# Kernel optimization log

Measured on AMD Instinct MI355X. Metric: run time of the kernel, lower is better.

Reference implementation:

```python
import jax, jax.numpy as jnp
import numpy as np

EMBED_SIZE = 512
SCALE = EMBED_SIZE ** 0.5  # note: sqrt(embed_size), not sqrt(head_dim), per source


def setup_inputs() -> dict:
    key = jax.random.key(0)
    kq, kk, kv = jax.random.split(key, 3)
    B, H, S, D = 4, 8, 2048, 64
    query = jax.random.normal(kq, (B, H, S, D), dtype=jnp.float32)
    key_t = jax.random.normal(kk, (B, H, S, D), dtype=jnp.float32)
    value = jax.random.normal(kv, (B, S, H, D), dtype=jnp.float32)  # [b, kv_len, h, d]
    return {"query": query, "key": key_t, "value": value}


def reference(query, key, value):
    # scores: [b, h, q, k]
    scores = jnp.einsum('bhqf,bhkf->bhqk', query, key)
    weight = jax.nn.softmax(scores / SCALE, axis=3)
    # value is [b, l, h, d]; output [b, q, h, d]
    out = jnp.einsum('bhql,blhd->bqhd', weight, value)
    return out
```

## Files before the change

### kernel.cpp

```cpp
#include <hip/hip_runtime.h>
#include <stdint.h>

#define NB 4
#define NH 8
#define NS 2048
#define ND 64
#define BQ 128
#define TK 64
#define KP 72
#define NG 2
#define NITG (NS/(TK*NG))
#define SLOT (TK*KP + ND*KP)

typedef __bf16  bf16x8 __attribute__((ext_vector_type(8)));
typedef float   f32x16 __attribute__((ext_vector_type(16)));

__device__ __forceinline__ uint32_t pkbf(float x, float y) {
  uint32_t ax = __builtin_bit_cast(uint32_t, x) + 0x8000u;
  uint32_t ay = __builtin_bit_cast(uint32_t, y) + 0x8000u;
  return __builtin_amdgcn_perm(ay, ax, 0x07060302u);
}
__device__ __forceinline__ unsigned short bfu(float x) {
  return (unsigned short)((__builtin_bit_cast(uint32_t, x) + 0x8000u) >> 16);
}

__global__ __launch_bounds__(512, 4) void fa_fwd(
    const float* __restrict__ Q, const float* __restrict__ K,
    const float* __restrict__ V, float* __restrict__ O)
{
  __shared__ __attribute__((aligned(16))) unsigned short SMEM[NG*2*SLOT];

  const int tid = threadIdx.x, wid = tid>>6, lane = tid&63;
  const int l31 = lane&31, h = lane>>5;
  const int g = wid>>2, qs = wid&3;
  const int tid4 = tid & 255;

  const int bid = blockIdx.x;
  const int logical = (bid & 7)*64 + (bid >> 3);
  const int bh = logical >> 4;
  const int q0 = (logical & 15) * BQ;
  const int b = bh>>3, hh = bh&7;

  const float* Qb = Q + ((size_t)bh*NS + q0)*ND;
  const float* Kb = K + (size_t)bh*NS*ND;
  const float* Vb = V + ((size_t)b*NS*NH + hh)*ND;
  float*       Ob = O + ((size_t)b*NS*NH + hh)*ND;

  const float kSc = 1.44269504088896340736f / 22.6274169979695207808f;

  bf16x8 qf[4];
  {
    const float* qp = Qb + (size_t)(qs*32 + l31)*ND + 8*h;
#pragma unroll
    for (int k=0;k<4;++k){
      float4 a = *(const float4*)(qp + 16*k);
      float4 c = *(const float4*)(qp + 16*k + 4);
      uint4 u = make_uint4(pkbf(a.x*kSc,a.y*kSc), pkbf(a.z*kSc,a.w*kSc),
                           pkbf(c.x*kSc,c.y*kSc), pkbf(c.z*kSc,c.w*kSc));
      qf[k] = __builtin_bit_cast(bf16x8, u);
    }
  }

  const int krow0 = tid4>>3, koct = tid&7;
  const int vq = lane&3, vrow = 16*qs + (lane>>2);

  float4 kst[2][2], vst[4];
  auto load_tile = [&](int kv0){
#pragma unroll
    for (int i=0;i<2;++i){
      const float* kp = Kb + (size_t)(kv0 + krow0 + 32*i)*ND + koct*8;
      kst[i][0] = *(const float4*)kp;
      kst[i][1] = *(const float4*)(kp+4);
    }
    const float* vp = Vb + (size_t)(kv0 + vrow)*(NH*ND) + 4*vq;
#pragma unroll
    for (int j=0;j<4;++j)
      vst[j] = *(const float4*)(vp + 16*j);
  };
  auto store_tile = [&](int buf){
    unsigned short* Kl = SMEM + (size_t)(g*2+buf)*SLOT;
    unsigned short* Vt = Kl + TK*KP;
#pragma unroll
    for (int i=0;i<2;++i){
      uint4 w = make_uint4(pkbf(kst[i][0].x,kst[i][0].y), pkbf(kst[i][0].z,kst[i][0].w),
                           pkbf(kst[i][1].x,kst[i][1].y), pkbf(kst[i][1].z,kst[i][1].w));
      *(uint4*)&Kl[(size_t)(krow0+32*i)*KP + koct*8] = w;
    }
#pragma unroll
    for (int j=0;j<4;++j){
      int d0 = 16*j + 4*vq;
      Vt[(size_t)(d0+0)*KP + vrow] = bfu(vst[j].x);
      Vt[(size_t)(d0+1)*KP + vrow] = bfu(vst[j].y);
      Vt[(size_t)(d0+2)*KP + vrow] = bfu(vst[j].z);
      Vt[(size_t)(d0+3)*KP + vrow] = bfu(vst[j].w);
    }
  };

  load_tile(g*NITG*TK);
  store_tile(0);
  __syncthreads();

  const f32x16 zero = {0,0,0,0,0,0,0,0,0,0,0,0,0,0,0,0};
  f32x16 acc[2] = {zero, zero};
  float lsum = 0.f;

  for (int t=0; t<NITG; ++t){
    const int cur = t&1;
    if (t+1 < NITG) load_tile((g*NITG + t + 1)*TK);

    const unsigned short* Kl = SMEM + (size_t)(g*2+cur)*SLOT;
    const unsigned short* Vt = Kl + TK*KP;

    f32x16 st[2];
    __builtin_amdgcn_s_setprio(1);
#pragma unroll
    for (int tt=0;tt<2;++tt){
      st[tt] = zero;
#pragma unroll
      for (int k=0;k<4;++k){
        bf16x8 kf = *(const bf16x8*)&Kl[(size_t)(32*tt+l31)*KP + 16*k + 8*h];
        st[tt] = __builtin_amdgcn_mfma_f32_32x32x16_bf16(kf, qf[k], st[tt], 0,0,0);
      }
    }
    __builtin_amdgcn_s_setprio(0);

    uint32_t P0[2][4], P1[2][4];
#pragma unroll
    for (int tt=0;tt<2;++tt)
#pragma unroll
      for (int u=0;u<4;++u){
        float p0 = __builtin_amdgcn_exp2f(st[tt][4*u+0]);
        float p1 = __builtin_amdgcn_exp2f(st[tt][4*u+1]);
        float p2 = __builtin_amdgcn_exp2f(st[tt][4*u+2]);
        float p3 = __builtin_amdgcn_exp2f(st[tt][4*u+3]);
        lsum += (p0+p1)+(p2+p3);
        P0[tt][u] = pkbf(p0,p1);
        P1[tt][u] = pkbf(p2,p3);
      }

    uint32_t X0[2][2], X1[2][2];
#pragma unroll
    for (int tt=0;tt<2;++tt)
#pragma unroll
      for (int m=0;m<2;++m){
        uint32_t y0 = h ? P0[tt][2*m] : P0[tt][2*m+1];
        uint32_t y1 = h ? P1[tt][2*m] : P1[tt][2*m+1];
        X0[tt][m] = (uint32_t)__shfl_xor((int)y0, 32, 64);
        X1[tt][m] = (uint32_t)__shfl_xor((int)y1, 32, 64);
      }
    bf16x8 pf[4];
#pragma unroll
    for (int k=0;k<4;++k){
      int tt = k>>1, m = k&1;
      uint32_t lo0 = h ? X0[tt][m]     : P0[tt][2*m];
      uint32_t lo1 = h ? X1[tt][m]     : P1[tt][2*m];
      uint32_t hi0 = h ? P0[tt][2*m+1] : X0[tt][m];
      uint32_t hi1 = h ? P1[tt][2*m+1] : X1[tt][m];
      uint4 u = make_uint4(lo0, lo1, hi0, hi1);
      pf[k] = __builtin_bit_cast(bf16x8, u);
    }

    __builtin_amdgcn_s_setprio(1);
#pragma unroll
    for (int gg=0;gg<2;++gg)
#pragma unroll
      for (int k=0;k<4;++k){
        bf16x8 vf = *(const bf16x8*)&Vt[(size_t)(32*gg+l31)*KP + 16*k + 8*h];
        acc[gg] = __builtin_amdgcn_mfma_f32_32x32x16_bf16(vf, pf[k], acc[gg], 0,0,0);
      }
    __builtin_amdgcn_s_setprio(0);

    if (t+1 < NITG) store_tile(cur^1);
    __syncthreads();
  }

  lsum += __shfl_xor(lsum, 32, 64);
  const int row = qs*32 + l31;
  float* accL = (float*)SMEM;
  float* lsL  = accL + 128*68;

  if (g==1){
#pragma unroll
    for (int gg=0; gg<2; ++gg)
#pragma unroll
      for (int u=0; u<4; ++u){
        float4 o;
        o.x = acc[gg][4*u+0]; o.y = acc[gg][4*u+1];
        o.z = acc[gg][4*u+2]; o.w = acc[gg][4*u+3];
        *(float4*)&accL[(size_t)row*68 + 32*gg + 8*u + 4*h] = o;
      }
    if (h==0) lsL[row] = lsum;
  }
  __syncthreads();
  if (g==0){
    const float inv = 1.0f/(lsum + lsL[row]);
    float* op = Ob + (size_t)(q0 + row)*(NH*ND);
#pragma unroll
    for (int gg=0; gg<2; ++gg)
#pragma unroll
      for (int u=0; u<4; ++u){
        float4 c = *(const float4*)&accL[(size_t)row*68 + 32*gg + 8*u + 4*h];
        float4 o;
        o.x = (acc[gg][4*u+0]+c.x)*inv;
        o.y = (acc[gg][4*u+1]+c.y)*inv;
        o.z = (acc[gg][4*u+2]+c.z)*inv;
        o.w = (acc[gg][4*u+3]+c.w)*inv;
        *(float4*)(op + 32*gg + 8*u + 4*h) = o;
      }
  }
}

extern "C" void kernel_launch(void* const* d_in, const int* in_sizes, int n_in,
                              void* d_out, int out_size, void* d_ws, size_t ws_size,
                              hipStream_t stream) {
  const float* Q = (const float*)d_in[0];
  const float* K = (const float*)d_in[1];
  const float* V = (const float*)d_in[2];
  float* O = (float*)d_out;
  dim3 grid((NS / BQ) * NB * NH);
  hipLaunchKernelGGL(fa_fwd, grid, dim3(512), 0, stream, Q, K, V, O);
}
```

Measured before the change: 149.6 us.

## Double query tile to 256 rows and split K/V staging across thread halves

Raises the query block to 256 rows with 1024-thread blocks, so each shared K/V tile in LDS is reused by 8 query strips per group instead of 4. This halves the global K/V reads and bf16 conversion work per query row. Tile loading is also rebalanced: within each group, one half of the threads stages K and the other half stages transposed V, instead of every thread doing both. The cost is half as many blocks (256), which may hurt load balance or latency hiding, plus larger blocks and a bigger epilogue reduction buffer in LDS.

```diff
diff --git a/kernel.cpp b/kernel.cpp
--- a/kernel.cpp
+++ b/kernel.cpp
@@ -5,7 +5,7 @@
 #define NH 8
 #define NS 2048
 #define ND 64
-#define BQ 128
+#define BQ 256
 #define TK 64
 #define KP 72
 #define NG 2
@@ -24,7 +24,7 @@
   return (unsigned short)((__builtin_bit_cast(uint32_t, x) + 0x8000u) >> 16);
 }
 
-__global__ __launch_bounds__(512, 4) void fa_fwd(
+__global__ __launch_bounds__(1024, 4) void fa_fwd(
     const float* __restrict__ Q, const float* __restrict__ K,
     const float* __restrict__ V, float* __restrict__ O)
 {
@@ -32,13 +32,15 @@
 
   const int tid = threadIdx.x, wid = tid>>6, lane = tid&63;
   const int l31 = lane&31, h = lane>>5;
-  const int g = wid>>2, qs = wid&3;
-  const int tid4 = tid & 255;
+  const int g = wid>>3, qs = wid&7;
+  const int tid9 = tid & 511;
+  const int sub = tid9 >> 8;
+  const int t4 = tid9 & 255;
 
   const int bid = blockIdx.x;
-  const int logical = (bid & 7)*64 + (bid >> 3);
-  const int bh = logical >> 4;
-  const int q0 = (logical & 15) * BQ;
+  const int logical = (bid & 7)*32 + (bid >> 3);
+  const int bh = logical >> 3;
+  const int q0 = (logical & 7) * BQ;
   const int b = bh>>3, hh = bh&7;
 
   const float* Qb = Q + ((size_t)bh*NS + q0)*ND;
@@ -61,38 +63,44 @@
     }
   }
 
-  const int krow0 = tid4>>3, koct = tid&7;
-  const int vq = lane&3, vrow = 16*qs + (lane>>2);
-
-  float4 kst[2][2], vst[4];
+  const int krow0 = t4>>3, koct = t4&7;
+  const int vrow = t4>>2, vq = t4&3;
+
+  float4 stg[4];
   auto load_tile = [&](int kv0){
-#pragma unroll
-    for (int i=0;i<2;++i){
-      const float* kp = Kb + (size_t)(kv0 + krow0 + 32*i)*ND + koct*8;
-      kst[i][0] = *(const float4*)kp;
-      kst[i][1] = *(const float4*)(kp+4);
-    }
-    const float* vp = Vb + (size_t)(kv0 + vrow)*(NH*ND) + 4*vq;
-#pragma unroll
-    for (int j=0;j<4;++j)
-      vst[j] = *(const float4*)(vp + 16*j);
+    if (sub==0){
+      const float* kp = Kb + (size_t)(kv0 + krow0)*ND + koct*8;
+      stg[0] = *(const float4*)kp;
+      stg[1] = *(const float4*)(kp+4);
+      const float* kp2 = kp + 32*ND;
+      stg[2] = *(const float4*)kp2;
+      stg[3] = *(const float4*)(kp2+4);
+    } else {
+      const float* vp = Vb + (size_t)(kv0 + vrow)*(NH*ND) + 4*vq;
+#pragma unroll
+      for (int j=0;j<4;++j)
+        stg[j] = *(const float4*)(vp + 16*j);
+    }
   };
   auto store_tile = [&](int buf){
     unsigned short* Kl = SMEM + (size_t)(g*2+buf)*SLOT;
     unsigned short* Vt = Kl + TK*KP;
-#pragma unroll
-    for (int i=0;i<2;++i){
-      uint4 w = make_uint4(pkbf(kst[i][0].x,kst[i][0].y), pkbf(kst[i][0].z,kst[i][0].w),
-                           pkbf(kst[i][1].x,kst[i][1].y), pkbf(kst[i][1].z,kst[i][1].w));
-      *(uint4*)&Kl[(size_t)(krow0+32*i)*KP + koct*8] = w;
-    }
-#pragma unroll
-    for (int j=0;j<4;++j){
-      int d0 = 16*j + 4*vq;
-      Vt[(size_t)(d0+0)*KP + vrow] = bfu(vst[j].x);
-      Vt[(size_t)(d0+1)*KP + vrow] = bfu(vst[j].y);
-      Vt[(size_t)(d0+2)*KP + vrow] = bfu(vst[j].z);
-      Vt[(size_t)(d0+3)*KP + vrow] = bfu(vst[j].w);
+    if (sub==0){
+      uint4 w0 = make_uint4(pkbf(stg[0].x,stg[0].y), pkbf(stg[0].z,stg[0].w),
+                            pkbf(stg[1].x,stg[1].y), pkbf(stg[1].z,stg[1].w));
+      *(uint4*)&Kl[(size_t)krow0*KP + koct*8] = w0;
+      uint4 w1 = make_uint4(pkbf(stg[2].x,stg[2].y), pkbf(stg[2].z,stg[2].w),
+                            pkbf(stg[3].x,stg[3].y), pkbf(stg[3].z,stg[3].w));
+      *(uint4*)&Kl[(size_t)(krow0+32)*KP + koct*8] = w1;
+    } else {
+#pragma unroll
+      for (int j=0;j<4;++j){
+        int d0 = 16*j + 4*vq;
+        Vt[(size_t)(d0+0)*KP + vrow] = bfu(stg[j].x);
+        Vt[(size_t)(d0+1)*KP + vrow] = bfu(stg[j].y);
+        Vt[(size_t)(d0+2)*KP + vrow] = bfu(stg[j].z);
+        Vt[(size_t)(d0+3)*KP + vrow] = bfu(stg[j].w);
+      }
     }
   };
 
@@ -177,7 +185,7 @@
   lsum += __shfl_xor(lsum, 32, 64);
   const int row = qs*32 + l31;
   float* accL = (float*)SMEM;
-  float* lsL  = accL + 128*68;
+  float* lsL  = accL + 256*68;
 
   if (g==1){
 #pragma unroll
@@ -218,5 +226,5 @@
   const float* V = (const float*)d_in[2];
   float* O = (float*)d_out;
   dim3 grid((NS / BQ) * NB * NH);
-  hipLaunchKernelGGL(fa_fwd, grid, dim3(512), 0, stream, Q, K, V, O);
-}
+  hipLaunchKernelGGL(fa_fwd, grid, dim3(1024), 0, stream, Q, K, V, O);
+}
```

Measured after the change: 170.4 us. +13.9%, slower.

## Precompute bf16 K and transposed bf16 V in a prep kernel

Applied to the files above, without the earlier changes.

Adds a pre-pass kernel that converts K to bf16 and writes V as bf16 transposed into a [b,h,d,s] workspace layout. The attention kernel then loads these half-width tiles with plain 16-byte vector loads and stores them straight to LDS, with no per-tile conversion or scattered transpose stores. This removes repeated fp32 K/V reads and conversion across the 16 query blocks per head. The cost is an extra kernel launch and a full pass over K and V plus workspace writes.

```diff
diff --git a/kernel.cpp b/kernel.cpp
--- a/kernel.cpp
+++ b/kernel.cpp
@@ -24,16 +24,60 @@
   return (unsigned short)((__builtin_bit_cast(uint32_t, x) + 0x8000u) >> 16);
 }
 
+__global__ __launch_bounds__(256) void prep(
+    const float* __restrict__ K, const float* __restrict__ V,
+    unsigned short* __restrict__ Kh, unsigned short* __restrict__ Vth)
+{
+  __shared__ unsigned short T[64*72];
+  const int t = threadIdx.x;
+  const int blk = blockIdx.x;
+  const int bh = blk >> 5, st = blk & 31;
+  const int s0 = st*64;
+  const int b = bh>>3, hh = bh&7;
+
+  {
+    const float* kin = K + ((size_t)bh*NS + s0)*ND + t*16;
+    unsigned short* kout = Kh + ((size_t)bh*NS + s0)*ND + t*16;
+    float4 a0 = ((const float4*)kin)[0], a1 = ((const float4*)kin)[1];
+    float4 a2 = ((const float4*)kin)[2], a3 = ((const float4*)kin)[3];
+    uint4 w0 = make_uint4(pkbf(a0.x,a0.y),pkbf(a0.z,a0.w),pkbf(a1.x,a1.y),pkbf(a1.z,a1.w));
+    uint4 w1 = make_uint4(pkbf(a2.x,a2.y),pkbf(a2.z,a2.w),pkbf(a3.x,a3.y),pkbf(a3.z,a3.w));
+    ((uint4*)kout)[0] = w0; ((uint4*)kout)[1] = w1;
+  }
+
+  {
+    const int vrow = t>>2, vq = t&3;
+    const float* vp = V + (((size_t)b*NS + s0 + vrow)*NH + hh)*ND + 4*vq;
+#pragma unroll
+    for (int j=0;j<4;++j){
+      float4 v = *(const float4*)(vp + 16*j);
+      int d0 = 16*j + 4*vq;
+      T[(size_t)(d0+0)*72 + vrow] = bfu(v.x);
+      T[(size_t)(d0+1)*72 + vrow] = bfu(v.y);
+      T[(size_t)(d0+2)*72 + vrow] = bfu(v.z);
+      T[(size_t)(d0+3)*72 + vrow] = bfu(v.w);
+    }
+  }
+  __syncthreads();
+  {
+    const int dd = t>>2, wq = t&3;
+    unsigned short* vout = Vth + ((size_t)bh*ND + dd)*NS + s0 + 16*wq;
+    uint4 o0 = *(const uint4*)&T[(size_t)dd*72 + 16*wq];
+    uint4 o1 = *(const uint4*)&T[(size_t)dd*72 + 16*wq + 8];
+    ((uint4*)vout)[0] = o0; ((uint4*)vout)[1] = o1;
+  }
+}
+
 __global__ __launch_bounds__(512, 4) void fa_fwd(
-    const float* __restrict__ Q, const float* __restrict__ K,
-    const float* __restrict__ V, float* __restrict__ O)
+    const float* __restrict__ Q, const unsigned short* __restrict__ Kh,
+    const unsigned short* __restrict__ Vth, float* __restrict__ O)
 {
   __shared__ __attribute__((aligned(16))) unsigned short SMEM[NG*2*SLOT];
 
   const int tid = threadIdx.x, wid = tid>>6, lane = tid&63;
   const int l31 = lane&31, h = lane>>5;
   const int g = wid>>2, qs = wid&3;
-  const int tid4 = tid & 255;
+  const int t4 = tid & 255;
 
   const int bid = blockIdx.x;
   const int logical = (bid & 7)*64 + (bid >> 3);
@@ -41,10 +85,10 @@
   const int q0 = (logical & 15) * BQ;
   const int b = bh>>3, hh = bh&7;
 
-  const float* Qb = Q + ((size_t)bh*NS + q0)*ND;
-  const float* Kb = K + (size_t)bh*NS*ND;
-  const float* Vb = V + ((size_t)b*NS*NH + hh)*ND;
-  float*       Ob = O + ((size_t)b*NS*NH + hh)*ND;
+  const float*          Qb  = Q   + ((size_t)bh*NS + q0)*ND;
+  const unsigned short* Kb  = Kh  + (size_t)bh*NS*ND;
+  const unsigned short* Vtb = Vth + (size_t)bh*ND*NS;
+  float*                Ob  = O   + ((size_t)b*NS*NH + hh)*ND;
 
   const float kSc = 1.44269504088896340736f / 22.6274169979695207808f;
 
@@ -61,39 +105,24 @@
     }
   }
 
-  const int krow0 = tid4>>3, koct = tid&7;
-  const int vq = lane&3, vrow = 16*qs + (lane>>2);
-
-  float4 kst[2][2], vst[4];
+  const int srow = t4>>3, soct = t4&7;
+
+  uint4 stg[4];
   auto load_tile = [&](int kv0){
-#pragma unroll
-    for (int i=0;i<2;++i){
-      const float* kp = Kb + (size_t)(kv0 + krow0 + 32*i)*ND + koct*8;
-      kst[i][0] = *(const float4*)kp;
-      kst[i][1] = *(const float4*)(kp+4);
-    }
-    const float* vp = Vb + (size_t)(kv0 + vrow)*(NH*ND) + 4*vq;
-#pragma unroll
-    for (int j=0;j<4;++j)
-      vst[j] = *(const float4*)(vp + 16*j);
+    const unsigned short* kp = Kb + (size_t)(kv0 + srow)*ND + 8*soct;
+    stg[0] = *(const uint4*)kp;
+    stg[1] = *(const uint4*)(kp + 32*ND);
+    const unsigned short* vp = Vtb + (size_t)srow*NS + kv0 + 8*soct;
+    stg[2] = *(const uint4*)vp;
+    stg[3] = *(const uint4*)(vp + (size_t)32*NS);
   };
   auto store_tile = [&](int buf){
     unsigned short* Kl = SMEM + (size_t)(g*2+buf)*SLOT;
     unsigned short* Vt = Kl + TK*KP;
-#pragma unroll
-    for (int i=0;i<2;++i){
-      uint4 w = make_uint4(pkbf(kst[i][0].x,kst[i][0].y), pkbf(kst[i][0].z,kst[i][0].w),
-                           pkbf(kst[i][1].x,kst[i][1].y), pkbf(kst[i][1].z,kst[i][1].w));
-      *(uint4*)&Kl[(size_t)(krow0+32*i)*KP + koct*8] = w;
-    }
-#pragma unroll
-    for (int j=0;j<4;++j){
-      int d0 = 16*j + 4*vq;
-      Vt[(size_t)(d0+0)*KP + vrow] = bfu(vst[j].x);
-      Vt[(size_t)(d0+1)*KP + vrow] = bfu(vst[j].y);
-      Vt[(size_t)(d0+2)*KP + vrow] = bfu(vst[j].z);
-      Vt[(size_t)(d0+3)*KP + vrow] = bfu(vst[j].w);
-    }
+    *(uint4*)&Kl[(size_t)srow*KP + 8*soct] = stg[0];
+    *(uint4*)&Kl[(size_t)(srow+32)*KP + 8*soct] = stg[1];
+    *(uint4*)&Vt[(size_t)srow*KP + 8*soct] = stg[2];
+    *(uint4*)&Vt[(size_t)(srow+32)*KP + 8*soct] = stg[3];
   };
 
   load_tile(g*NITG*TK);
@@ -217,6 +246,9 @@
   const float* K = (const float*)d_in[1];
   const float* V = (const float*)d_in[2];
   float* O = (float*)d_out;
+  unsigned short* Kh  = (unsigned short*)d_ws;
+  unsigned short* Vth = Kh + (size_t)NB*NH*NS*ND;
+  hipLaunchKernelGGL(prep, dim3(NB*NH*(NS/64)), dim3(256), 0, stream, K, V, Kh, Vth);
   dim3 grid((NS / BQ) * NB * NH);
-  hipLaunchKernelGGL(fa_fwd, grid, dim3(512), 0, stream, Q, K, V, O);
-}
+  hipLaunchKernelGGL(fa_fwd, grid, dim3(512), 0, stream, Q, Kh, Vth, O);
+}
```

Measured after the change: 158.2 us. 1.06x slower.

## Use permlane32 swap for P redistribution and reshape V tile loading

Applied to the files above, without the earlier changes.

Replaces the shfl_xor plus per-lane select exchange of softmax probabilities with the gfx950 permlane32_swap instruction, which swaps register halves between the two 32-lane groups without going through LDS bpermute. It also changes the V global load pattern so each lane loads one kv row with strided column groups, and the transposed LDS stores are indexed by lane. The V change alters global coalescing (each lane reads a different row, 16B per row segment) and LDS bank patterns, which may help or hurt. Correctness depends on permlane32_swap semantics matching the previous select logic.

```diff
diff --git a/kernel.cpp b/kernel.cpp
--- a/kernel.cpp
+++ b/kernel.cpp
@@ -24,6 +24,14 @@
   return (unsigned short)((__builtin_bit_cast(uint32_t, x) + 0x8000u) >> 16);
 }
 
+__device__ __forceinline__ void plswap(uint32_t a, uint32_t b,
+                                       uint32_t& lo, uint32_t& hi) {
+  auto r = __builtin_amdgcn_permlane32_swap(a, b, false, false);
+  uint64_t p = __builtin_bit_cast(uint64_t, r);
+  lo = (uint32_t)p;
+  hi = (uint32_t)(p >> 32);
+}
+
 __global__ __launch_bounds__(512, 4) void fa_fwd(
     const float* __restrict__ Q, const float* __restrict__ K,
     const float* __restrict__ V, float* __restrict__ O)
@@ -62,20 +70,18 @@
   }
 
   const int krow0 = tid4>>3, koct = tid&7;
-  const int vq = lane&3, vrow = 16*qs + (lane>>2);
 
   float4 kst[2][2], vst[4];
-  auto load_tile = [&](int kv0){
+  auto load_tile = [&](int kb){
 #pragma unroll
     for (int i=0;i<2;++i){
-      const float* kp = Kb + (size_t)(kv0 + krow0 + 32*i)*ND + koct*8;
+      const float* kp = Kb + (size_t)(kb + krow0 + 32*i)*ND + koct*8;
       kst[i][0] = *(const float4*)kp;
       kst[i][1] = *(const float4*)(kp+4);
     }
-    const float* vp = Vb + (size_t)(kv0 + vrow)*(NH*ND) + 4*vq;
-#pragma unroll
-    for (int j=0;j<4;++j)
-      vst[j] = *(const float4*)(vp + 16*j);
+#pragma unroll
+    for (int i=0;i<4;++i)
+      vst[i] = *(const float4*)(Vb + (size_t)(kb + lane)*(NH*ND) + (qs+4*i)*4);
   };
   auto store_tile = [&](int buf){
     unsigned short* Kl = SMEM + (size_t)(g*2+buf)*SLOT;
@@ -87,12 +93,12 @@
       *(uint4*)&Kl[(size_t)(krow0+32*i)*KP + koct*8] = w;
     }
 #pragma unroll
-    for (int j=0;j<4;++j){
-      int d0 = 16*j + 4*vq;
-      Vt[(size_t)(d0+0)*KP + vrow] = bfu(vst[j].x);
-      Vt[(size_t)(d0+1)*KP + vrow] = bfu(vst[j].y);
-      Vt[(size_t)(d0+2)*KP + vrow] = bfu(vst[j].z);
-      Vt[(size_t)(d0+3)*KP + vrow] = bfu(vst[j].w);
+    for (int i=0;i<4;++i){
+      int d0 = (qs+4*i)*4;
+      Vt[(size_t)(d0+0)*KP + lane] = bfu(vst[i].x);
+      Vt[(size_t)(d0+1)*KP + lane] = bfu(vst[i].y);
+      Vt[(size_t)(d0+2)*KP + lane] = bfu(vst[i].z);
+      Vt[(size_t)(d0+3)*KP + lane] = bfu(vst[i].w);
     }
   };
 
@@ -138,24 +144,13 @@
         P1[tt][u] = pkbf(p2,p3);
       }
 
-    uint32_t X0[2][2], X1[2][2];
-#pragma unroll
-    for (int tt=0;tt<2;++tt)
-#pragma unroll
-      for (int m=0;m<2;++m){
-        uint32_t y0 = h ? P0[tt][2*m] : P0[tt][2*m+1];
-        uint32_t y1 = h ? P1[tt][2*m] : P1[tt][2*m+1];
-        X0[tt][m] = (uint32_t)__shfl_xor((int)y0, 32, 64);
-        X1[tt][m] = (uint32_t)__shfl_xor((int)y1, 32, 64);
-      }
     bf16x8 pf[4];
 #pragma unroll
     for (int k=0;k<4;++k){
       int tt = k>>1, m = k&1;
-      uint32_t lo0 = h ? X0[tt][m]     : P0[tt][2*m];
-      uint32_t lo1 = h ? X1[tt][m]     : P1[tt][2*m];
-      uint32_t hi0 = h ? P0[tt][2*m+1] : X0[tt][m];
-      uint32_t hi1 = h ? P1[tt][2*m+1] : X1[tt][m];
+      uint32_t lo0, hi0, lo1, hi1;
+      plswap(P0[tt][2*m], P0[tt][2*m+1], lo0, hi0);
+      plswap(P1[tt][2*m], P1[tt][2*m+1], lo1, hi1);
       uint4 u = make_uint4(lo0, lo1, hi0, hi1);
       pf[k] = __builtin_bit_cast(bf16x8, u);
     }
```

Result: no change. 151.8 us (+1.5%).
